# Kernel tuning notes

Measured on AMD Instinct MI355X. Metric: run time of the kernel, lower is better.

The kernel has to match this reference:

```python
import jax, jax.numpy as jnp
import numpy as np

# Dimensions: B tokens, D=d_model, H=4*D expert hidden, E experts, K=top_k
B, D, H, E, K = 2048, 1024, 4096, 8, 2


def setup_inputs() -> dict:
    key = jax.random.key(0)
    ks = jax.random.split(key, 5)
    scale = 0.02
    return {
        "moe_inp": jax.random.normal(ks[0], (B, D), jnp.float32),
        # NaiveGate: single Linear(d_model -> num_expert)
        "gate_w": jax.random.normal(ks[1], (E, D), jnp.float32) * scale,
        "gate_b": jnp.zeros((E,), jnp.float32),
        # Fused experts: per-expert htoh4 (D->H) and h4toh (H->D).
        # Stored pre-transposed relative to torch Linear.weight for x @ W.
        "w1": jax.random.normal(ks[2], (E, D, H), jnp.float32) * scale,
        "b1": jnp.zeros((E, H), jnp.float32),
        "w2": jax.random.normal(ks[3], (E, H, D), jnp.float32) * scale,
        "b2": jnp.zeros((E, D), jnp.float32),
    }


def reference(moe_inp, gate_w, gate_b, w1, b1, w2, b2):
    # --- NaiveGate: linear -> top-k -> softmax over selected logits ---
    logits = moe_inp @ gate_w.T + gate_b            # [B, E]
    top_val, top_idx = jax.lax.top_k(logits, K)     # [B, K]
    gate_score = jax.nn.softmax(top_val, axis=-1)   # [B, K]

    # --- Grouped expert FFN (all experts on all tokens; combine weights
    #     are zero for non-selected experts so the math matches exact
    #     token dispatch + per-expert GEMM + weighted bmm combine) ---
    h = jnp.einsum('bd,edh->ebh', moe_inp, w1) + b1[:, None, :]   # [E, B, H]
    h = jax.nn.gelu(h, approximate=False)
    y = jnp.einsum('ebh,ehd->ebd', h, w2) + b2[:, None, :]        # [E, B, D]

    # combine weight per (token, expert): sum of gate scores of matching top-k slots
    combine = jnp.sum(jax.nn.one_hot(top_idx, E, dtype=moe_inp.dtype)
                      * gate_score[..., None], axis=1)            # [B, E]
    out = jnp.einsum('be,ebd->bd', combine, y)                    # [B, D]
    return out
```

## Files before the change

kernel.cpp:

```cpp
#include <hip/hip_runtime.h>
#include <math.h>

#define B_TOK 2048
#define DMODEL 1024
#define HDIM 4096
#define NEXP 8
#define TOPK 2

#define BM 128
#define BK 64
#define MAX_TILES 40
#define MAX_T256 24

typedef __attribute__((ext_vector_type(8))) short bf16x8;
typedef __attribute__((ext_vector_type(4))) float f32x4;

__device__ __forceinline__ unsigned short f2b(float f) {
  unsigned u = __builtin_bit_cast(unsigned, f);
  unsigned r = (u + 0x7FFFu + ((u >> 16) & 1u)) >> 16;
  return (unsigned short)r;
}

__device__ __forceinline__ void load_lds16(const void* g, void* l) {
  __builtin_amdgcn_global_load_lds(
      (const __attribute__((address_space(1))) unsigned int*)g,
      (__attribute__((address_space(3))) unsigned int*)l, 16, 0, 0);
}

__device__ __forceinline__ float gelu_fast(float v) {
  float x = v * 0.70710678118654752f;
  float ax = fabsf(x);
  float t = 1.0f / (1.0f + 0.3275911f * ax);
  float e = exp2f(-ax * ax * 1.4426950408889634f);
  float p = t * (0.254829592f +
                 t * (-0.284496736f +
                      t * (1.421413741f +
                           t * (-1.453152027f + t * 1.061405429f))));
  float er = 1.0f - p * e;
  er = copysignf(er, x);
  return 0.5f * v * (1.0f + er);
}

__global__ __launch_bounds__(256) void gate_kernel(
    const float* __restrict__ x, const float* __restrict__ gw,
    const float* __restrict__ gb, int* __restrict__ idx2,
    float* __restrict__ sc2, float* __restrict__ out) {
  int lane = threadIdx.x & 63;
  int w = threadIdx.x >> 6;
  int b = blockIdx.x * 4 + w;
  {
    float4 z = make_float4(0.f, 0.f, 0.f, 0.f);
    float* orow = out + (size_t)(blockIdx.x * 4) * DMODEL;
#pragma unroll
    for (int i = 0; i < 4; ++i)
      *(float4*)(orow + i * 1024 + threadIdx.x * 4) = z;
  }
  double acc[NEXP];
#pragma unroll
  for (int e = 0; e < NEXP; ++e) acc[e] = 0.0;
  const float* xr = x + (size_t)b * DMODEL;
#pragma unroll
  for (int i = 0; i < 4; ++i) {
    float4 xv = *(const float4*)(xr + i * 256 + lane * 4);
#pragma unroll
    for (int e = 0; e < NEXP; ++e) {
      float4 wv = *(const float4*)(gw + e * DMODEL + i * 256 + lane * 4);
      acc[e] += (double)xv.x * wv.x + (double)xv.y * wv.y +
                (double)xv.z * wv.z + (double)xv.w * wv.w;
    }
  }
#pragma unroll
  for (int e = 0; e < NEXP; ++e) {
    double v = acc[e];
    for (int o = 1; o < 64; o <<= 1) v += __shfl_xor(v, o, 64);
    acc[e] = v + (double)gb[e];
  }
  if (lane == 0) {
    int i0 = 0;
    double v0 = acc[0];
#pragma unroll
    for (int e = 1; e < NEXP; ++e)
      if (acc[e] > v0) { v0 = acc[e]; i0 = e; }
    int i1 = -1;
    double v1 = -1e300;
#pragma unroll
    for (int e = 0; e < NEXP; ++e)
      if (e != i0 && acc[e] > v1) { v1 = acc[e]; i1 = e; }
    double t = exp(v1 - v0);
    float s0 = (float)(1.0 / (1.0 + t));
    float s1 = (float)(t / (1.0 + t));
    idx2[b * 2] = i0;
    idx2[b * 2 + 1] = i1;
    sc2[b * 2] = s0;
    sc2[b * 2 + 1] = s1;
  }
}

__global__ __launch_bounds__(256) void route_kernel(
    const int* __restrict__ idx2, const float* __restrict__ sc2,
    int* __restrict__ tile_map, int* __restrict__ ntiles,
    int* __restrict__ tm256, int* __restrict__ nt256,
    int* __restrict__ pos_of, int* __restrict__ row_of,
    float* __restrict__ s_of) {
  __shared__ int lc[NEXP][257];
  __shared__ int offs[NEXP + 1];
  const int tid = threadIdx.x;
  const int base = tid * 16;
#pragma unroll
  for (int e = 0; e < NEXP; ++e) lc[e][tid + 1] = 0;
  if (tid < NEXP) lc[tid][0] = 0;
  __syncthreads();
  int loc[16];
#pragma unroll
  for (int j = 0; j < 16; ++j) {
    int e = idx2[base + j];
    loc[j] = e;
    atomicAdd(&lc[e][tid + 1], 1);
  }
  __syncthreads();
  if (tid < NEXP) {
    int s = 0;
    for (int i = 1; i <= 256; ++i) {
      s += lc[tid][i];
      lc[tid][i] = s;
    }
  }
  __syncthreads();
  if (tid == 0) {
    offs[0] = 0;
    for (int e = 0; e < NEXP; ++e) offs[e + 1] = offs[e] + lc[e][256];
    int tt = 0, t2 = 0;
    for (int e = 0; e < NEXP; ++e) {
      int cnt = lc[e][256];
      int bse = offs[e];
      for (int t = 0; t * BM < cnt; ++t) {
        tile_map[tt * 4 + 0] = e;
        tile_map[tt * 4 + 1] = bse + t * BM;
        tile_map[tt * 4 + 2] = (cnt - t * BM) < BM ? (cnt - t * BM) : BM;
        tile_map[tt * 4 + 3] = 0;
        ++tt;
      }
      for (int t = 0; t * 256 < cnt; ++t) {
        tm256[t2 * 4 + 0] = e;
        tm256[t2 * 4 + 1] = bse + t * 256;
        tm256[t2 * 4 + 2] = (cnt - t * 256) < 256 ? (cnt - t * 256) : 256;
        tm256[t2 * 4 + 3] = 0;
        ++t2;
      }
    }
    *ntiles = tt;
    *nt256 = t2;
  }
  __syncthreads();
#pragma unroll
  for (int e = 0; e < NEXP; ++e) lc[e][tid] += offs[e];
  __syncthreads();
#pragma unroll
  for (int j = 0; j < 16; ++j) {
    int e = loc[j];
    int p = lc[e][tid];
    lc[e][tid] = p + 1;
    int t = base + j;
    pos_of[t] = p;
    row_of[p] = t >> 1;
    s_of[p] = sc2[t];
  }
}

__global__ __launch_bounds__(256) void gather_kernel(
    const float* __restrict__ x, const int* __restrict__ row_of,
    unsigned short* __restrict__ Xp) {
  int r = blockIdx.x;
  int tok = row_of[r];
  int c = threadIdx.x * 4;
  float4 v = *(const float4*)(x + (size_t)tok * DMODEL + c);
  ushort4 o = make_ushort4(f2b(v.x), f2b(v.y), f2b(v.z), f2b(v.w));
  *(ushort4*)(Xp + (size_t)r * DMODEL + c) = o;
}

__global__ __launch_bounds__(256) void convT_kernel(
    const float* __restrict__ W, unsigned short* __restrict__ Wt, int Kd, int Nd,
    int tilesN, int cpx) {
  __shared__ unsigned L[64 * 33];
  int bidx = (blockIdx.x & 7) * cpx + (blockIdx.x >> 3);
  int nt = bidx % tilesN;
  int r2 = bidx / tilesN;
  int tilesK = Kd >> 6;
  int kt = r2 % tilesK;
  int e = r2 / tilesK;
  int tid = threadIdx.x;

  const float* src = W + (long)e * Kd * Nd + (long)(kt * 64) * Nd + nt * 64;
  int kp = tid >> 3;
  int nb = tid & 7;
  const float* r0 = src + (long)(2 * kp) * Nd + nb * 8;
  const float* r1 = r0 + Nd;
  float4 va0 = *(const float4*)r0;
  float4 va1 = *(const float4*)(r0 + 4);
  float4 vb0 = *(const float4*)r1;
  float4 vb1 = *(const float4*)(r1 + 4);
  const float* a = (const float*)&va0;
  const float* bq = (const float*)&vb0;
#pragma unroll
  for (int j = 0; j < 4; ++j) {
    unsigned p = (unsigned)f2b(a[j]) | ((unsigned)f2b(bq[j]) << 16);
    L[(nb * 8 + j) * 33 + kp] = p;
  }
  const float* a2 = (const float*)&va1;
  const float* b2 = (const float*)&vb1;
#pragma unroll
  for (int j = 0; j < 4; ++j) {
    unsigned p = (unsigned)f2b(a2[j]) | ((unsigned)f2b(b2[j]) << 16);
    L[(nb * 8 + 4 + j) * 33 + kp] = p;
  }
  __syncthreads();
  int n = tid >> 2;
  int part = tid & 3;
  unsigned q[8];
#pragma unroll
  for (int j = 0; j < 8; ++j) q[j] = L[n * 33 + part * 8 + j];
  unsigned* dst = (unsigned*)(Wt + (long)e * Nd * Kd + (long)(nt * 64 + n) * Kd +
                              kt * 64) +
                  part * 8;
  *(uint4*)dst = make_uint4(q[0], q[1], q[2], q[3]);
  *(uint4*)(dst + 4) = make_uint4(q[4], q[5], q[6], q[7]);
}

__global__ __launch_bounds__(512) void gemm1_wide(
    const unsigned short* __restrict__ A, int lda,
    const unsigned short* __restrict__ Bt, long strideB,
    const float* __restrict__ bias, unsigned short* __restrict__ Cout, int ldc,
    const int* __restrict__ tm256, const int* __restrict__ nt256, int N,
    int K) {
  const int nb = N / 128;
  const int tile = blockIdx.x / nb;
  if (tile >= *nt256) return;
  const int ct = blockIdx.x % nb;
  const int e = tm256[tile * 4 + 0];
  const int row0 = tm256[tile * 4 + 1];
  const int rows = tm256[tile * 4 + 2];
  const int n0 = ct * 128;
  const unsigned short* B_e = Bt + (long)e * strideB + (long)n0 * K;

  __shared__ __align__(16) unsigned short Asm[256 * BK];
  __shared__ __align__(16) unsigned short Bsm[128 * BK];

  const int tid = threadIdx.x;
  const int lane = tid & 63;
  const int w = tid >> 6;
  const int wr = (w >> 1) * 64;
  const int wc = (w & 1) * 64;
  const int l15 = lane & 15;
  const int l4 = lane >> 4;

  f32x4 acc[4][4] = {};

  for (int k0 = 0; k0 < K; k0 += BK) {
#pragma unroll
    for (int it = 0; it < 4; ++it) {
      int c = it * 512 + tid;
      int r = c >> 3, kc = c & 7;
      int kcs = kc ^ (r & 7);
      load_lds16(A + (size_t)(row0 + r) * lda + k0 + kcs * 8,
                 ((char*)Asm) + (size_t)(it * 512 + w * 64) * 16);
    }
#pragma unroll
    for (int it = 0; it < 2; ++it) {
      int c = it * 512 + tid;
      int r = c >> 3, kc = c & 7;
      int kcs = kc ^ (r & 7);
      load_lds16(B_e + (size_t)r * K + k0 + kcs * 8,
                 ((char*)Bsm) + (size_t)(it * 512 + w * 64) * 16);
    }
    __syncthreads();
#pragma unroll
    for (int kk = 0; kk < 2; ++kk) {
      bf16x8 a[4], b[4];
#pragma unroll
      for (int m = 0; m < 4; ++m) {
        int row = wr + m * 16 + l15;
        int ch = (kk * 4 + l4) ^ (l15 & 7);
        a[m] = *(const bf16x8*)&Asm[row * BK + ch * 8];
      }
#pragma unroll
      for (int n = 0; n < 4; ++n) {
        int row = wc + n * 16 + l15;
        int ch = (kk * 4 + l4) ^ (l15 & 7);
        b[n] = *(const bf16x8*)&Bsm[row * BK + ch * 8];
      }
#pragma unroll
      for (int m = 0; m < 4; ++m)
#pragma unroll
        for (int n = 0; n < 4; ++n)
          acc[m][n] =
              __builtin_amdgcn_mfma_f32_16x16x32_bf16(a[m], b[n], acc[m][n], 0, 0, 0);
    }
    __syncthreads();
  }

  const float* bias_e = bias + (long)e * HDIM;
#pragma unroll
  for (int m = 0; m < 4; ++m) {
#pragma unroll
    for (int i = 0; i < 4; ++i) {
      int r = wr + m * 16 + l4 * 4 + i;
      if (r < rows) {
        size_t grow = (size_t)(row0 + r) * ldc;
#pragma unroll
        for (int n = 0; n < 4; ++n) {
          int cg = n0 + wc + n * 16 + l15;
          float v = acc[m][n][i] + bias_e[cg];
          v = gelu_fast(v);
          Cout[grow + cg] = f2b(v);
        }
      }
    }
  }
}

__global__ __launch_bounds__(256) void gemm2_db(
    const unsigned short* __restrict__ A,
    const unsigned short* __restrict__ Bt,
    const float* __restrict__ bias, float* __restrict__ out,
    const int* __restrict__ row_of, const float* __restrict__ s_of,
    const int* __restrict__ tile_map, const int* __restrict__ ntiles) {
  const int K = HDIM, N = DMODEL;
  const int nb = N / 64;
  const int tile = blockIdx.x / nb;
  if (tile >= *ntiles) return;
  const int ct = blockIdx.x % nb;
  const int e = tile_map[tile * 4 + 0];
  const int row0 = tile_map[tile * 4 + 1];
  const int rows = tile_map[tile * 4 + 2];
  const int n0 = ct * 64;
  const unsigned short* B_e = Bt + (long)e * N * K + (long)n0 * K;

  __shared__ __align__(16) unsigned short Asm[2][BM * BK];
  __shared__ __align__(16) unsigned short Bsm[2][64 * BK];

  const int tid = threadIdx.x;
  const int lane = tid & 63;
  const int w = tid >> 6;
  const int wr = w * 32;
  const int l15 = lane & 15;
  const int l4 = lane >> 4;
  const int rA = tid >> 3, kcA = tid & 7;

  f32x4 acc[2][4] = {};

#define STAGE2D(buf, k0)                                                      \
  {                                                                           \
    _Pragma("unroll") for (int it = 0; it < 4; ++it) {                        \
      int r = it * 32 + rA;                                                   \
      int kcs = kcA ^ (r & 7);                                                \
      load_lds16(A + (size_t)(row0 + r) * K + (k0) + kcs * 8,                 \
                 ((char*)Asm[buf]) + (size_t)(it * 256 + w * 64) * 16);       \
    }                                                                         \
    _Pragma("unroll") for (int it = 0; it < 2; ++it) {                        \
      int r = it * 32 + rA;                                                   \
      int kcs = kcA ^ (r & 7);                                                \
      load_lds16(B_e + (size_t)r * K + (k0) + kcs * 8,                        \
                 ((char*)Bsm[buf]) + (size_t)(it * 256 + w * 64) * 16);       \
    }                                                                         \
  }

#define COMPUTE2D(buf)                                                        \
  {                                                                           \
    _Pragma("unroll") for (int kk = 0; kk < 2; ++kk) {                        \
      bf16x8 a[2], b[4];                                                      \
      _Pragma("unroll") for (int m = 0; m < 2; ++m) {                         \
        int row = wr + m * 16 + l15;                                          \
        int ch = (kk * 4 + l4) ^ (l15 & 7);                                   \
        a[m] = *(const bf16x8*)&Asm[buf][row * BK + ch * 8];                  \
      }                                                                       \
      _Pragma("unroll") for (int n = 0; n < 4; ++n) {                         \
        int row = n * 16 + l15;                                               \
        int ch = (kk * 4 + l4) ^ (l15 & 7);                                   \
        b[n] = *(const bf16x8*)&Bsm[buf][row * BK + ch * 8];                  \
      }                                                                       \
      _Pragma("unroll") for (int m = 0; m < 2; ++m)                           \
          _Pragma("unroll") for (int n = 0; n < 4; ++n) acc[m][n] =           \
              __builtin_amdgcn_mfma_f32_16x16x32_bf16(a[m], b[n], acc[m][n],  \
                                                      0, 0, 0);               \
    }                                                                         \
  }

  const int nsteps = K / BK;
  STAGE2D(0, 0);
  STAGE2D(1, BK);
#pragma unroll 1
  for (int t = 0; t < nsteps - 1; ++t) {
    asm volatile("s_waitcnt vmcnt(6)" ::: "memory");
    __builtin_amdgcn_s_barrier();
    COMPUTE2D(t & 1);
    __builtin_amdgcn_s_barrier();
    if (t + 2 < nsteps) STAGE2D(t & 1, (t + 2) * BK);
  }
  asm volatile("s_waitcnt vmcnt(0)" ::: "memory");
  __builtin_amdgcn_s_barrier();
  COMPUTE2D((nsteps - 1) & 1);
#undef STAGE2D
#undef COMPUTE2D

  const float* bias_e = bias + (long)e * DMODEL;
#pragma unroll
  for (int m = 0; m < 2; ++m) {
#pragma unroll
    for (int i = 0; i < 4; ++i) {
      int r = wr + m * 16 + l4 * 4 + i;
      if (r < rows) {
        int tok = row_of[row0 + r];
        float s = s_of[row0 + r];
        float* op = out + (size_t)tok * DMODEL;
#pragma unroll
        for (int n = 0; n < 4; ++n) {
          int cg = n0 + n * 16 + l15;
          float v = acc[m][n][i] + bias_e[cg];
          atomicAdd(&op[cg], s * v);
        }
      }
    }
  }
}

extern "C" void kernel_launch(void* const* d_in, const int* in_sizes, int n_in,
                              void* d_out, int out_size, void* d_ws, size_t ws_size,
                              hipStream_t stream) {
  const float* x = (const float*)d_in[0];
  const float* gw = (const float*)d_in[1];
  const float* gb = (const float*)d_in[2];
  const float* w1 = (const float*)d_in[3];
  const float* b1 = (const float*)d_in[4];
  const float* w2 = (const float*)d_in[5];
  const float* b2 = (const float*)d_in[6];
  float* out = (float*)d_out;
  char* ws = (char*)d_ws;

  int* ntiles = (int*)(ws + 128);
  int* nt256 = (int*)(ws + 132);
  int* tile_map = (int*)(ws + 256);
  int* tm256 = (int*)(ws + 2048);
  int* idx2 = (int*)(ws + 4096);
  float* sc2 = (float*)(ws + 20480);
  int* pos_of = (int*)(ws + 36864);
  int* row_of = (int*)(ws + 53248);
  float* s_of = (float*)(ws + 73728);
  unsigned short* Xp = (unsigned short*)(ws + 131072);
  unsigned short* H1 = (unsigned short*)(ws + 8781824);
  unsigned short* Wt = (unsigned short*)(ws + 43384832);
  if (ws_size < 110493696ULL) return;

  gate_kernel<<<B_TOK / 4, 256, 0, stream>>>(x, gw, gb, idx2, sc2, out);
  route_kernel<<<1, 256, 0, stream>>>(idx2, sc2, tile_map, ntiles, tm256, nt256,
                                      pos_of, row_of, s_of);
  gather_kernel<<<B_TOK * TOPK, 256, 0, stream>>>(x, row_of, Xp);

  convT_kernel<<<NEXP * (DMODEL / 64) * (HDIM / 64), 256, 0, stream>>>(
      w1, Wt, DMODEL, HDIM, HDIM / 64, NEXP * (DMODEL / 64) * (HDIM / 64) / 8);
  gemm1_wide<<<MAX_T256 * (HDIM / 128), 512, 0, stream>>>(
      Xp, DMODEL, Wt, (long)HDIM * DMODEL, b1, H1, HDIM, tm256, nt256, HDIM,
      DMODEL);
  convT_kernel<<<NEXP * (HDIM / 64) * (DMODEL / 64), 256, 0, stream>>>(
      w2, Wt, HDIM, DMODEL, DMODEL / 64, NEXP * (HDIM / 64) * (DMODEL / 64) / 8);
  gemm2_db<<<MAX_TILES * (DMODEL / 64), 256, 0, stream>>>(
      H1, Wt, b2, out, row_of, s_of, tile_map, ntiles);
}
```

Measured before the change: 269.3 us.

## Replace wide 256-row gemm1 with 128-row tiles and XCD-aware block swizzle

The first expert GEMM now uses 128-row token tiles from the existing tile_map with 256-thread blocks, dropping the separate 256-row tile list. Block indices are remapped so that each XCD (blockIdx mod 8) handles a contiguous group of up to five row tiles across all column tiles. The aim is to keep the same A rows and expert weights in one XCD's L2 and to balance work across XCDs. The cost is more blocks and a lower per-block reuse ratio (128x128 instead of 256x128). The launch assumes at most 40 tiles, and the tile split only fits that grid while ntiles/8 rounds up to at most 5.

```diff
diff --git a/kernel.cpp b/kernel.cpp
--- a/kernel.cpp
+++ b/kernel.cpp
@@ -99,7 +99,6 @@
 __global__ __launch_bounds__(256) void route_kernel(
     const int* __restrict__ idx2, const float* __restrict__ sc2,
     int* __restrict__ tile_map, int* __restrict__ ntiles,
-    int* __restrict__ tm256, int* __restrict__ nt256,
     int* __restrict__ pos_of, int* __restrict__ row_of,
     float* __restrict__ s_of) {
   __shared__ int lc[NEXP][257];
@@ -129,7 +128,7 @@
   if (tid == 0) {
     offs[0] = 0;
     for (int e = 0; e < NEXP; ++e) offs[e + 1] = offs[e] + lc[e][256];
-    int tt = 0, t2 = 0;
+    int tt = 0;
     for (int e = 0; e < NEXP; ++e) {
       int cnt = lc[e][256];
       int bse = offs[e];
@@ -140,16 +139,8 @@
         tile_map[tt * 4 + 3] = 0;
         ++tt;
       }
-      for (int t = 0; t * 256 < cnt; ++t) {
-        tm256[t2 * 4 + 0] = e;
-        tm256[t2 * 4 + 1] = bse + t * 256;
-        tm256[t2 * 4 + 2] = (cnt - t * 256) < 256 ? (cnt - t * 256) : 256;
-        tm256[t2 * 4 + 3] = 0;
-        ++t2;
-      }
     }
     *ntiles = tt;
-    *nt256 = t2;
   }
   __syncthreads();
 #pragma unroll
@@ -226,23 +217,29 @@
   *(uint4*)(dst + 4) = make_uint4(q[4], q[5], q[6], q[7]);
 }
 
-__global__ __launch_bounds__(512) void gemm1_wide(
-    const unsigned short* __restrict__ A, int lda,
-    const unsigned short* __restrict__ Bt, long strideB,
-    const float* __restrict__ bias, unsigned short* __restrict__ Cout, int ldc,
-    const int* __restrict__ tm256, const int* __restrict__ nt256, int N,
-    int K) {
+__global__ __launch_bounds__(256) void gemm1_swz(
+    const unsigned short* __restrict__ A,
+    const unsigned short* __restrict__ Bt,
+    const float* __restrict__ bias, unsigned short* __restrict__ Cout,
+    const int* __restrict__ tile_map, const int* __restrict__ ntiles) {
+  const int K = DMODEL, N = HDIM;
   const int nb = N / 128;
-  const int tile = blockIdx.x / nb;
-  if (tile >= *nt256) return;
-  const int ct = blockIdx.x % nb;
-  const int e = tm256[tile * 4 + 0];
-  const int row0 = tm256[tile * 4 + 1];
-  const int rows = tm256[tile * 4 + 2];
+  const int xcd = blockIdx.x & 7;
+  const int slot = blockIdx.x >> 3;
+  const int lt = slot % 5;
+  const int ct = slot / 5;
+  const int nt = *ntiles;
+  const int q = nt >> 3, r = nt & 7;
+  const int cnt = q + (xcd < r ? 1 : 0);
+  if (lt >= cnt) return;
+  const int tile = (xcd < r ? xcd * (q + 1) : r * (q + 1) + (xcd - r) * q) + lt;
+  const int e = tile_map[tile * 4 + 0];
+  const int row0 = tile_map[tile * 4 + 1];
+  const int rows = tile_map[tile * 4 + 2];
   const int n0 = ct * 128;
-  const unsigned short* B_e = Bt + (long)e * strideB + (long)n0 * K;
-
-  __shared__ __align__(16) unsigned short Asm[256 * BK];
+  const unsigned short* B_e = Bt + (long)e * N * K + (long)n0 * K;
+
+  __shared__ __align__(16) unsigned short Asm[BM * BK];
   __shared__ __align__(16) unsigned short Bsm[128 * BK];
 
   const int tid = threadIdx.x;
@@ -258,19 +255,19 @@
   for (int k0 = 0; k0 < K; k0 += BK) {
 #pragma unroll
     for (int it = 0; it < 4; ++it) {
-      int c = it * 512 + tid;
-      int r = c >> 3, kc = c & 7;
-      int kcs = kc ^ (r & 7);
-      load_lds16(A + (size_t)(row0 + r) * lda + k0 + kcs * 8,
-                 ((char*)Asm) + (size_t)(it * 512 + w * 64) * 16);
-    }
-#pragma unroll
-    for (int it = 0; it < 2; ++it) {
-      int c = it * 512 + tid;
-      int r = c >> 3, kc = c & 7;
-      int kcs = kc ^ (r & 7);
-      load_lds16(B_e + (size_t)r * K + k0 + kcs * 8,
-                 ((char*)Bsm) + (size_t)(it * 512 + w * 64) * 16);
+      int c = it * 256 + tid;
+      int rr = c >> 3, kc = c & 7;
+      int kcs = kc ^ (rr & 7);
+      load_lds16(A + (size_t)(row0 + rr) * K + k0 + kcs * 8,
+                 ((char*)Asm) + (size_t)(it * 256 + w * 64) * 16);
+    }
+#pragma unroll
+    for (int it = 0; it < 4; ++it) {
+      int c = it * 256 + tid;
+      int rr = c >> 3, kc = c & 7;
+      int kcs = kc ^ (rr & 7);
+      load_lds16(B_e + (size_t)rr * K + k0 + kcs * 8,
+                 ((char*)Bsm) + (size_t)(it * 256 + w * 64) * 16);
     }
     __syncthreads();
 #pragma unroll
@@ -303,9 +300,9 @@
   for (int m = 0; m < 4; ++m) {
 #pragma unroll
     for (int i = 0; i < 4; ++i) {
-      int r = wr + m * 16 + l4 * 4 + i;
-      if (r < rows) {
-        size_t grow = (size_t)(row0 + r) * ldc;
+      int rr = wr + m * 16 + l4 * 4 + i;
+      if (rr < rows) {
+        size_t grow = (size_t)(row0 + rr) * HDIM;
 #pragma unroll
         for (int n = 0; n < 4; ++n) {
           int cg = n0 + wc + n * 16 + l15;
@@ -437,9 +434,7 @@
   char* ws = (char*)d_ws;
 
   int* ntiles = (int*)(ws + 128);
-  int* nt256 = (int*)(ws + 132);
   int* tile_map = (int*)(ws + 256);
-  int* tm256 = (int*)(ws + 2048);
   int* idx2 = (int*)(ws + 4096);
   float* sc2 = (float*)(ws + 20480);
   int* pos_of = (int*)(ws + 36864);
@@ -451,15 +446,14 @@
   if (ws_size < 110493696ULL) return;
 
   gate_kernel<<<B_TOK / 4, 256, 0, stream>>>(x, gw, gb, idx2, sc2, out);
-  route_kernel<<<1, 256, 0, stream>>>(idx2, sc2, tile_map, ntiles, tm256, nt256,
-                                      pos_of, row_of, s_of);
+  route_kernel<<<1, 256, 0, stream>>>(idx2, sc2, tile_map, ntiles, pos_of,
+                                      row_of, s_of);
   gather_kernel<<<B_TOK * TOPK, 256, 0, stream>>>(x, row_of, Xp);
 
   convT_kernel<<<NEXP * (DMODEL / 64) * (HDIM / 64), 256, 0, stream>>>(
       w1, Wt, DMODEL, HDIM, HDIM / 64, NEXP * (DMODEL / 64) * (HDIM / 64) / 8);
-  gemm1_wide<<<MAX_T256 * (HDIM / 128), 512, 0, stream>>>(
-      Xp, DMODEL, Wt, (long)HDIM * DMODEL, b1, H1, HDIM, tm256, nt256, HDIM,
-      DMODEL);
+  gemm1_swz<<<8 * 5 * (HDIM / 128), 256, 0, stream>>>(Xp, Wt, b1, H1, tile_map,
+                                                      ntiles);
   convT_kernel<<<NEXP * (HDIM / 64) * (DMODEL / 64), 256, 0, stream>>>(
       w2, Wt, HDIM, DMODEL, DMODEL / 64, NEXP * (HDIM / 64) * (DMODEL / 64) / 8);
   gemm2_db<<<MAX_TILES * (DMODEL / 64), 256, 0, stream>>>(
```

Measured after the change: 270.5 us. Within noise of the previous version (+0.4%).

## Fuse gate with W1 conversion and gather rows inside GEMM1 loads

Applied to the files above, without the earlier changes.

Merges the gate kernel and the first weight transpose/convert into one launch, and has the gate side write a bf16 copy of the input. The separate gather kernel is removed: GEMM1 now looks up row_of per tile and loads the token rows straight from the bf16 input. This is meant to cut two kernel launches and one gathered activation copy, at the cost of indirect row addresses in the GEMM A loads. Route also zeroes padding entries of row_of so padded tile rows point at a valid token.

```diff
diff --git a/kernel.cpp b/kernel.cpp
--- a/kernel.cpp
+++ b/kernel.cpp
@@ -41,58 +41,109 @@
   return 0.5f * v * (1.0f + er);
 }
 
-__global__ __launch_bounds__(256) void gate_kernel(
+__global__ __launch_bounds__(256) void gate_conv_kernel(
     const float* __restrict__ x, const float* __restrict__ gw,
     const float* __restrict__ gb, int* __restrict__ idx2,
-    float* __restrict__ sc2, float* __restrict__ out) {
-  int lane = threadIdx.x & 63;
-  int w = threadIdx.x >> 6;
-  int b = blockIdx.x * 4 + w;
-  {
-    float4 z = make_float4(0.f, 0.f, 0.f, 0.f);
-    float* orow = out + (size_t)(blockIdx.x * 4) * DMODEL;
-#pragma unroll
-    for (int i = 0; i < 4; ++i)
-      *(float4*)(orow + i * 1024 + threadIdx.x * 4) = z;
-  }
-  double acc[NEXP];
-#pragma unroll
-  for (int e = 0; e < NEXP; ++e) acc[e] = 0.0;
-  const float* xr = x + (size_t)b * DMODEL;
-#pragma unroll
-  for (int i = 0; i < 4; ++i) {
-    float4 xv = *(const float4*)(xr + i * 256 + lane * 4);
+    float* __restrict__ sc2, float* __restrict__ out,
+    unsigned short* __restrict__ x16, const float* __restrict__ W,
+    unsigned short* __restrict__ Wt) {
+  __shared__ unsigned L[64 * 33];
+  if (blockIdx.x < 512) {
+    int lane = threadIdx.x & 63;
+    int w = threadIdx.x >> 6;
+    int b = blockIdx.x * 4 + w;
+    {
+      float4 z = make_float4(0.f, 0.f, 0.f, 0.f);
+      float* orow = out + (size_t)(blockIdx.x * 4) * DMODEL;
+#pragma unroll
+      for (int i = 0; i < 4; ++i)
+        *(float4*)(orow + i * 1024 + threadIdx.x * 4) = z;
+    }
+    double acc[NEXP];
+#pragma unroll
+    for (int e = 0; e < NEXP; ++e) acc[e] = 0.0;
+    const float* xr = x + (size_t)b * DMODEL;
+#pragma unroll
+    for (int i = 0; i < 4; ++i) {
+      float4 xv = *(const float4*)(xr + i * 256 + lane * 4);
+      ushort4 o = make_ushort4(f2b(xv.x), f2b(xv.y), f2b(xv.z), f2b(xv.w));
+      *(ushort4*)(x16 + (size_t)b * DMODEL + i * 256 + lane * 4) = o;
+#pragma unroll
+      for (int e = 0; e < NEXP; ++e) {
+        float4 wv = *(const float4*)(gw + e * DMODEL + i * 256 + lane * 4);
+        acc[e] += (double)xv.x * wv.x + (double)xv.y * wv.y +
+                  (double)xv.z * wv.z + (double)xv.w * wv.w;
+      }
+    }
 #pragma unroll
     for (int e = 0; e < NEXP; ++e) {
-      float4 wv = *(const float4*)(gw + e * DMODEL + i * 256 + lane * 4);
-      acc[e] += (double)xv.x * wv.x + (double)xv.y * wv.y +
-                (double)xv.z * wv.z + (double)xv.w * wv.w;
-    }
-  }
-#pragma unroll
-  for (int e = 0; e < NEXP; ++e) {
-    double v = acc[e];
-    for (int o = 1; o < 64; o <<= 1) v += __shfl_xor(v, o, 64);
-    acc[e] = v + (double)gb[e];
-  }
-  if (lane == 0) {
-    int i0 = 0;
-    double v0 = acc[0];
-#pragma unroll
-    for (int e = 1; e < NEXP; ++e)
-      if (acc[e] > v0) { v0 = acc[e]; i0 = e; }
-    int i1 = -1;
-    double v1 = -1e300;
-#pragma unroll
-    for (int e = 0; e < NEXP; ++e)
-      if (e != i0 && acc[e] > v1) { v1 = acc[e]; i1 = e; }
-    double t = exp(v1 - v0);
-    float s0 = (float)(1.0 / (1.0 + t));
-    float s1 = (float)(t / (1.0 + t));
-    idx2[b * 2] = i0;
-    idx2[b * 2 + 1] = i1;
-    sc2[b * 2] = s0;
-    sc2[b * 2 + 1] = s1;
+      double v = acc[e];
+      for (int o = 1; o < 64; o <<= 1) v += __shfl_xor(v, o, 64);
+      acc[e] = v + (double)gb[e];
+    }
+    if (lane == 0) {
+      int i0 = 0;
+      double v0 = acc[0];
+#pragma unroll
+      for (int e = 1; e < NEXP; ++e)
+        if (acc[e] > v0) { v0 = acc[e]; i0 = e; }
+      int i1 = -1;
+      double v1 = -1e300;
+#pragma unroll
+      for (int e = 0; e < NEXP; ++e)
+        if (e != i0 && acc[e] > v1) { v1 = acc[e]; i1 = e; }
+      double t = exp(v1 - v0);
+      float s0 = (float)(1.0 / (1.0 + t));
+      float s1 = (float)(t / (1.0 + t));
+      idx2[b * 2] = i0;
+      idx2[b * 2 + 1] = i1;
+      sc2[b * 2] = s0;
+      sc2[b * 2 + 1] = s1;
+    }
+  } else {
+    int bid0 = blockIdx.x - 512;
+    int bidx = (bid0 & 7) * 1024 + (bid0 >> 3);
+    int nt = bidx % (HDIM / 64);
+    int r2 = bidx / (HDIM / 64);
+    int kt = r2 % (DMODEL / 64);
+    int e = r2 / (DMODEL / 64);
+    int tid = threadIdx.x;
+
+    const float* src =
+        W + (long)e * DMODEL * HDIM + (long)(kt * 64) * HDIM + nt * 64;
+    int kp = tid >> 3;
+    int nb = tid & 7;
+    const float* r0 = src + (long)(2 * kp) * HDIM + nb * 8;
+    const float* r1 = r0 + HDIM;
+    float4 va0 = *(const float4*)r0;
+    float4 va1 = *(const float4*)(r0 + 4);
+    float4 vb0 = *(const float4*)r1;
+    float4 vb1 = *(const float4*)(r1 + 4);
+    const float* a = (const float*)&va0;
+    const float* bq = (const float*)&vb0;
+#pragma unroll
+    for (int j = 0; j < 4; ++j) {
+      unsigned p = (unsigned)f2b(a[j]) | ((unsigned)f2b(bq[j]) << 16);
+      L[(nb * 8 + j) * 33 + kp] = p;
+    }
+    const float* a2 = (const float*)&va1;
+    const float* b2 = (const float*)&vb1;
+#pragma unroll
+    for (int j = 0; j < 4; ++j) {
+      unsigned p = (unsigned)f2b(a2[j]) | ((unsigned)f2b(b2[j]) << 16);
+      L[(nb * 8 + 4 + j) * 33 + kp] = p;
+    }
+    __syncthreads();
+    int n = tid >> 2;
+    int part = tid & 3;
+    unsigned q[8];
+#pragma unroll
+    for (int j = 0; j < 8; ++j) q[j] = L[n * 33 + part * 8 + j];
+    unsigned* dst = (unsigned*)(Wt + (long)e * HDIM * DMODEL +
+                                (long)(nt * 64 + n) * DMODEL + kt * 64) +
+                    part * 8;
+    *(uint4*)dst = make_uint4(q[0], q[1], q[2], q[3]);
+    *(uint4*)(dst + 4) = make_uint4(q[4], q[5], q[6], q[7]);
   }
 }
 
@@ -106,6 +157,7 @@
   __shared__ int offs[NEXP + 1];
   const int tid = threadIdx.x;
   const int base = tid * 16;
+  row_of[4096 + tid] = 0;
 #pragma unroll
   for (int e = 0; e < NEXP; ++e) lc[e][tid + 1] = 0;
   if (tid < NEXP) lc[tid][0] = 0;
@@ -167,17 +219,6 @@
   }
 }
 
-__global__ __launch_bounds__(256) void gather_kernel(
-    const float* __restrict__ x, const int* __restrict__ row_of,
-    unsigned short* __restrict__ Xp) {
-  int r = blockIdx.x;
-  int tok = row_of[r];
-  int c = threadIdx.x * 4;
-  float4 v = *(const float4*)(x + (size_t)tok * DMODEL + c);
-  ushort4 o = make_ushort4(f2b(v.x), f2b(v.y), f2b(v.z), f2b(v.w));
-  *(ushort4*)(Xp + (size_t)r * DMODEL + c) = o;
-}
-
 __global__ __launch_bounds__(256) void convT_kernel(
     const float* __restrict__ W, unsigned short* __restrict__ Wt, int Kd, int Nd,
     int tilesN, int cpx) {
@@ -227,7 +268,7 @@
 }
 
 __global__ __launch_bounds__(512) void gemm1_wide(
-    const unsigned short* __restrict__ A, int lda,
+    const unsigned short* __restrict__ x16, const int* __restrict__ row_of,
     const unsigned short* __restrict__ Bt, long strideB,
     const float* __restrict__ bias, unsigned short* __restrict__ Cout, int ldc,
     const int* __restrict__ tm256, const int* __restrict__ nt256, int N,
@@ -253,15 +294,17 @@
   const int l15 = lane & 15;
   const int l4 = lane >> 4;
 
+  int gr[4];
+#pragma unroll
+  for (int it = 0; it < 4; ++it) gr[it] = row_of[row0 + it * 64 + (tid >> 3)];
+  const int kcsA = (tid & 7) ^ ((tid >> 3) & 7);
+
   f32x4 acc[4][4] = {};
 
   for (int k0 = 0; k0 < K; k0 += BK) {
 #pragma unroll
     for (int it = 0; it < 4; ++it) {
-      int c = it * 512 + tid;
-      int r = c >> 3, kc = c & 7;
-      int kcs = kc ^ (r & 7);
-      load_lds16(A + (size_t)(row0 + r) * lda + k0 + kcs * 8,
+      load_lds16(x16 + (size_t)gr[it] * K + k0 + kcsA * 8,
                  ((char*)Asm) + (size_t)(it * 512 + w * 64) * 16);
     }
 #pragma unroll
@@ -445,20 +488,17 @@
   int* pos_of = (int*)(ws + 36864);
   int* row_of = (int*)(ws + 53248);
   float* s_of = (float*)(ws + 73728);
-  unsigned short* Xp = (unsigned short*)(ws + 131072);
+  unsigned short* x16 = (unsigned short*)(ws + 131072);
   unsigned short* H1 = (unsigned short*)(ws + 8781824);
   unsigned short* Wt = (unsigned short*)(ws + 43384832);
   if (ws_size < 110493696ULL) return;
 
-  gate_kernel<<<B_TOK / 4, 256, 0, stream>>>(x, gw, gb, idx2, sc2, out);
+  gate_conv_kernel<<<512 + NEXP * (DMODEL / 64) * (HDIM / 64), 256, 0, stream>>>(
+      x, gw, gb, idx2, sc2, out, x16, w1, Wt);
   route_kernel<<<1, 256, 0, stream>>>(idx2, sc2, tile_map, ntiles, tm256, nt256,
                                       pos_of, row_of, s_of);
-  gather_kernel<<<B_TOK * TOPK, 256, 0, stream>>>(x, row_of, Xp);
-
-  convT_kernel<<<NEXP * (DMODEL / 64) * (HDIM / 64), 256, 0, stream>>>(
-      w1, Wt, DMODEL, HDIM, HDIM / 64, NEXP * (DMODEL / 64) * (HDIM / 64) / 8);
   gemm1_wide<<<MAX_T256 * (HDIM / 128), 512, 0, stream>>>(
-      Xp, DMODEL, Wt, (long)HDIM * DMODEL, b1, H1, HDIM, tm256, nt256, HDIM,
+      x16, row_of, Wt, (long)HDIM * DMODEL, b1, H1, HDIM, tm256, nt256, HDIM,
       DMODEL);
   convT_kernel<<<NEXP * (HDIM / 64) * (DMODEL / 64), 256, 0, stream>>>(
       w2, Wt, HDIM, DMODEL, DMODEL / 64, NEXP * (HDIM / 64) * (DMODEL / 64) / 8);
```

After: 253.1 us. 6.0% less time.
